# Optimization experiments

Hardware: AMD Instinct MI355X
Metric: run time of the kernel (lower is better)

## Reference

```python
import jax, jax.numpy as jnp
import numpy as np

N, E, G = 100000, 600000, 64  # nodes, edges, graphs
F_IN, W, EPS = 32, 128, 1e-5


def setup_inputs() -> dict:
    key = jax.random.key(0)
    ks = jax.random.split(key, 16)
    p = lambda k, shape: jax.random.normal(k, shape, dtype=jnp.float32) * 0.1
    z = lambda n: jnp.zeros((n,), jnp.float32)
    o = lambda n: jnp.ones((n,), jnp.float32)
    return {
        "x": jax.random.normal(ks[0], (N, F_IN), dtype=jnp.float32),
        "edge_index": jax.random.randint(ks[1], (2, E), 0, N, dtype=jnp.int32),
        "batch": jnp.sort(jax.random.randint(ks[2], (N,), 0, G, dtype=jnp.int32)),
        # GCNConv layers
        "W1": p(ks[3], (F_IN, W)), "b1": z(W),
        "W2": p(ks[4], (W, W)), "b2": z(W),
        # mlp_first: Linear -> BN -> ReLU -> Linear
        "W3": p(ks[5], (W, W)), "b3": z(W), "g1": o(W), "be1": z(W),
        "W4": p(ks[6], (W, W)), "b4": z(W),
        # mlp: Linear -> BN -> ReLU -> Linear
        "W5": p(ks[7], (W, W // 2)), "b5": z(W // 2), "g2": o(W // 2), "be2": z(W // 2),
        "W6": p(ks[8], (W // 2, 1)), "b6": z(1),
    }


def gcn_conv(x, src, dst, Wt, b):
    # PyG GCNConv with add_self_loops=True: D^-1/2 (A+I) D^-1/2 (x W) + b
    h = x @ Wt  # [N, width]
    deg = jax.ops.segment_sum(jnp.ones(src.shape[0], x.dtype), dst, num_segments=N) + 1.0
    dinv = jax.lax.rsqrt(deg)
    norm = dinv[src] * dinv[dst]  # per-edge normalization
    agg = jax.ops.segment_sum(h[src] * norm[:, None], dst, num_segments=N)
    # self-loop term: norm for (i,i) is 1/deg[i]
    return agg + h * (dinv * dinv)[:, None] + b


def batch_norm(x, g, b):
    # training-mode BatchNorm1d (batch stats, biased var)
    mu = x.mean(axis=0)
    var = jnp.mean((x - mu) ** 2, axis=0)
    return (x - mu) * jax.lax.rsqrt(var + EPS) * g + b


def reference(x, edge_index, batch, W1, b1, W2, b2, W3, b3, g1, be1, W4, b4, W5, b5, g2, be2, W6, b6):
    src, dst = edge_index[0], edge_index[1]
    x = jax.nn.relu(gcn_conv(x, src, dst, W1, b1))
    x = jax.nn.relu(gcn_conv(x, src, dst, W2, b2))
    # mlp_first + ReLU
    x = jax.nn.relu(batch_norm(x @ W3 + b3, g1, be1)) @ W4 + b4
    x = jax.nn.relu(x)
    # global max pool over nodes per graph
    x = jax.ops.segment_max(x, batch, num_segments=G)  # [G, width]
    # final mlp
    x = jax.nn.relu(batch_norm(x @ W5 + b5, g2, be2)) @ W6 + b6
    return x[:, 0]
```

## Files before the change

### kernel.cpp

```cpp
#include <hip/hip_runtime.h>

#define N_NODES 100000
#define N_EDGES 600000
#define N_GRAPHS 64
#define EPS 1e-5f
#define SCAN_BLOCKS 391

typedef unsigned short u16;
typedef unsigned int u32;
typedef __attribute__((ext_vector_type(8))) short bf16x8;
typedef __attribute__((ext_vector_type(4))) float f32x4;

__device__ __forceinline__ float bf2f(u16 u) { return __uint_as_float(((u32)u) << 16); }
__device__ __forceinline__ u16 f2bf(float f) {
    u32 u = __float_as_uint(f);
    u += 0x7FFFu + ((u >> 16) & 1u);
    return (u16)(u >> 16);
}
__device__ __forceinline__ float2 bfx2(u32 v) {
    float2 r;
    r.x = __uint_as_float(v << 16);
    r.y = __uint_as_float(v & 0xFFFF0000u);
    return r;
}

#define WS_COUNTS   ((size_t)0)
#define WS_CURSOR   ((size_t)400384)
#define WS_POOLED   ((size_t)800768)
#define WS_BNSUM    ((size_t)833536)
#define WS_BNSUMSQ  ((size_t)834048)
#define WS_FLAG     ((size_t)834560)
#define ZERO_BYTES  ((size_t)835072)
#define WS_OFFSETS  ((size_t)835072)
#define WS_DINV     ((size_t)1235456)
#define WS_DINV2    ((size_t)1635840)
#define WS_SRCS     ((size_t)2036224)
#define WS_ZF       ((size_t)4436736)
#define WS_CANONW   ((size_t)4453120)
#define WS_BUFA     ((size_t)4578560)
#define WS_BUFB     ((size_t)30178560)

#define CW_W1 0
#define CW_B1 4096
#define CW_W2 4224
#define CW_B2 20608
#define CW_W3 20736
#define CW_B3 37120
#define CW_G1 37248
#define CW_BE1 37376
#define CW_W4 37504
#define CW_B4 53888
#define CW_W5 54016
#define CW_B5 62208
#define CW_G2 62272
#define CW_BE2 62336
#define CW_W6 62400
#define CW_B6 62464

__global__ void detect_kernel(const u32* __restrict__ xraw, int* __restrict__ flag) {
    __shared__ int cnt;
    if (threadIdx.x == 0) cnt = 0;
    __syncthreads();
    int c = 0;
    for (int i = threadIdx.x; i < 2048; i += 256) {
        u32 w = xraw[i];
        float a = fabsf(__uint_as_float((w & 0xFFFFu) << 16));
        if (a == 0.f || (a > 1e-8f && a < 1e4f)) c++;
    }
    atomicAdd(&cnt, c);
    __syncthreads();
    if (threadIdx.x == 0) *flag = (cnt > 1024) ? 1 : 0;
}

__global__ void convx_kernel(const void* __restrict__ xsrc, u16* __restrict__ dst,
                             const int* __restrict__ flag) {
    int i = blockIdx.x * 256 + threadIdx.x;
    if (i < N_NODES * 32)
        dst[i] = (*flag) ? ((const u16*)xsrc)[i] : f2bf(((const float*)xsrc)[i]);
}

struct SmallArgs {
    const void* src[16];
    int n[16];
    int off[16];
    int cols[16];
};
__global__ void convs_kernel(SmallArgs a, u16* __restrict__ dst, const int* __restrict__ flag) {
    int i = blockIdx.x * 256 + threadIdx.x;
    int isbf = *flag;
#pragma unroll
    for (int j = 0; j < 16; j++)
        if (i < a.n[j]) {
            u16 v = isbf ? ((const u16*)a.src[j])[i] : f2bf(((const float*)a.src[j])[i]);
            if (a.cols[j] > 0) {
                int k = i / a.cols[j];
                int n = i - k * a.cols[j];
                int Kd = a.n[j] / a.cols[j];
                dst[a.off[j] + n * Kd + k] = v;
            } else {
                dst[a.off[j] + i] = v;
            }
        }
}

__global__ void deg_kernel(const int* __restrict__ dst, int* __restrict__ counts) {
    int e = blockIdx.x * 256 + threadIdx.x;
    if (e < N_EDGES) atomicAdd(&counts[dst[e]], 1);
}

__global__ __launch_bounds__(256) void reduce_kernel(const int* __restrict__ counts,
                                                     int* __restrict__ partials) {
    int i = blockIdx.x * 256 + threadIdx.x;
    int v = (i < N_NODES) ? counts[i] : 0;
    for (int off = 32; off > 0; off >>= 1) v += __shfl_down(v, off, 64);
    __shared__ int wsum[4];
    if ((threadIdx.x & 63) == 0) wsum[threadIdx.x >> 6] = v;
    __syncthreads();
    if (threadIdx.x == 0) partials[blockIdx.x] = wsum[0] + wsum[1] + wsum[2] + wsum[3];
}

__global__ __launch_bounds__(512) void scanpart_kernel(int* __restrict__ partials) {
    __shared__ int sc[512];
    int t = threadIdx.x;
    int v = (t < SCAN_BLOCKS) ? partials[t] : 0;
    sc[t] = v;
    __syncthreads();
    for (int off = 1; off < 512; off <<= 1) {
        int u = (t >= off) ? sc[t - off] : 0;
        __syncthreads();
        sc[t] += u;
        __syncthreads();
    }
    if (t < SCAN_BLOCKS) partials[t] = sc[t] - v;
}

__global__ __launch_bounds__(256) void offsets_kernel(const int* __restrict__ counts,
                                                      const int* __restrict__ partials,
                                                      int* __restrict__ offs,
                                                      float* __restrict__ dinv) {
    int i = blockIdx.x * 256 + threadIdx.x;
    int lane = threadIdx.x & 63, wv = threadIdx.x >> 6;
    int v = (i < N_NODES) ? counts[i] : 0;
    int sv = v;
    for (int off = 1; off < 64; off <<= 1) {
        int u = __shfl_up(sv, off, 64);
        if (lane >= off) sv += u;
    }
    __shared__ int wsum[4];
    if (lane == 63) wsum[wv] = sv;
    __syncthreads();
    int wpre = 0;
    for (int w = 0; w < wv; w++) wpre += wsum[w];
    int excl = sv - v + wpre + partials[blockIdx.x];
    if (i < N_NODES) {
        offs[i] = excl;
        dinv[i] = rsqrtf((float)(v + 1));
    }
    if (i == N_NODES - 1) offs[N_NODES] = excl + v;
}

__global__ void scatter_kernel(const int* __restrict__ src, const int* __restrict__ dst,
                               const int* __restrict__ offs, int* __restrict__ cursor,
                               int* __restrict__ srcs) {
    int e = blockIdx.x * 256 + threadIdx.x;
    if (e < N_EDGES) {
        int d = dst[e];
        int p = offs[d] + atomicAdd(&cursor[d], 1);
        srcs[p] = src[e];
    }
}

template <int K, int IN_MODE, int OUT_MODE>
__global__ __launch_bounds__(256, 3) void mgemm_kernel(
    const u16* __restrict__ A, const u16* __restrict__ Wt, const u16* __restrict__ bias,
    u16* __restrict__ C, const float* __restrict__ scl, const float* __restrict__ shf,
    const float* __restrict__ dscale, float* __restrict__ bn_sum,
    float* __restrict__ bn_sumsq, const int* __restrict__ batch, u32* __restrict__ pooled,
    const int* __restrict__ goffs, const int* __restrict__ gsrcs,
    const float* __restrict__ gdinv, const u16* __restrict__ gbias, int M) {
    constexpr int KP = K + 8;
    constexpr int NKT = K / 32;
    __shared__ __align__(16) u16 Wl[128 * KP];
    __shared__ float csum[128], csumsq[128];

    const int tid = threadIdx.x;
    const int wave = tid >> 6;
    const int lane = tid & 63;
    const int l15 = lane & 15;
    const int quad = lane >> 4;
    const int row0 = blockIdx.x * 128 + wave * 32;

    {
        const u32* g = (const u32*)Wt;
        u32* l = (u32*)Wl;
        for (int i = tid; i < 128 * (K / 2); i += 256) {
            int n = i / (K / 2), j = i - n * (K / 2);
            l[n * (KP / 2) + j] = g[i];
        }
    }
    if (OUT_MODE == 1 && tid < 128) { csum[tid] = 0.f; csumsq[tid] = 0.f; }

    uint4 gr[2][NKT];
    if (IN_MODE == 2) {
#pragma unroll
        for (int rt = 0; rt < 2; rt++) {
            int r = min(row0 + rt * 16 + l15, M - 1);
            int e0 = goffs[r], e1 = goffs[r + 1];
            float ga[NKT][8];
#pragma unroll
            for (int kt = 0; kt < NKT; kt++)
#pragma unroll
                for (int j = 0; j < 8; j++) ga[kt][j] = 0.f;
            for (int e = e0; e < e1; e++) {
                int s = gsrcs[e];
                const u16* hp = A + (size_t)s * K + quad * 8;
#pragma unroll
                for (int kt = 0; kt < NKT; kt++) {
                    uint4 raw = *(const uint4*)(hp + kt * 32);
                    u32 w4[4] = {raw.x, raw.y, raw.z, raw.w};
#pragma unroll
                    for (int t = 0; t < 4; t++) {
                        float2 f = bfx2(w4[t]);
                        ga[kt][2 * t] += f.x;
                        ga[kt][2 * t + 1] += f.y;
                    }
                }
            }
            float di = gdinv[r];
            const u16* op = A + (size_t)r * K + quad * 8;
#pragma unroll
            for (int kt = 0; kt < NKT; kt++) {
                uint4 own = *(const uint4*)(op + kt * 32);
                uint4 bb = *(const uint4*)(gbias + kt * 32 + quad * 8);
                u32 ow[4] = {own.x, own.y, own.z, own.w};
                u32 bw[4] = {bb.x, bb.y, bb.z, bb.w};
                u32 pk[4];
#pragma unroll
                for (int t = 0; t < 4; t++) {
                    float2 fo = bfx2(ow[t]);
                    float2 fb = bfx2(bw[t]);
                    float vx = fmaxf(fmaf(ga[kt][2 * t] + fo.x, di, fb.x), 0.f);
                    float vy = fmaxf(fmaf(ga[kt][2 * t + 1] + fo.y, di, fb.y), 0.f);
                    pk[t] = (u32)f2bf(vx) | ((u32)f2bf(vy) << 16);
                }
                gr[rt][kt] = {pk[0], pk[1], pk[2], pk[3]};
            }
        }
    }
    __syncthreads();

    f32x4 acc[2][8];
#pragma unroll
    for (int rt = 0; rt < 2; rt++)
#pragma unroll
        for (int nt = 0; nt < 8; nt++) acc[rt][nt] = {0.f, 0.f, 0.f, 0.f};

#pragma unroll
    for (int k0 = 0; k0 < K; k0 += 32) {
        bf16x8 af[2];
        if (IN_MODE == 2) {
#pragma unroll
            for (int rt = 0; rt < 2; rt++) af[rt] = __builtin_bit_cast(bf16x8, gr[rt][k0 / 32]);
        } else if (IN_MODE == 0) {
#pragma unroll
            for (int rt = 0; rt < 2; rt++) {
                int r = min(row0 + rt * 16 + l15, M - 1);
                af[rt] = *(const bf16x8*)(A + (size_t)r * K + k0 + quad * 8);
            }
        } else {
            float s8[8], h8[8];
#pragma unroll
            for (int t = 0; t < 8; t++) {
                s8[t] = scl[k0 + quad * 8 + t];
                h8[t] = shf[k0 + quad * 8 + t];
            }
#pragma unroll
            for (int rt = 0; rt < 2; rt++) {
                int r = min(row0 + rt * 16 + l15, M - 1);
                uint4 raw = *(const uint4*)(A + (size_t)r * K + k0 + quad * 8);
                u32 w4[4] = {raw.x, raw.y, raw.z, raw.w};
                bf16x8 tmp;
#pragma unroll
                for (int t = 0; t < 4; t++) {
                    float2 f = bfx2(w4[t]);
                    f.x = fmaxf(fmaf(f.x, s8[2 * t], h8[2 * t]), 0.f);
                    f.y = fmaxf(fmaf(f.y, s8[2 * t + 1], h8[2 * t + 1]), 0.f);
                    tmp[2 * t] = (short)f2bf(f.x);
                    tmp[2 * t + 1] = (short)f2bf(f.y);
                }
                af[rt] = tmp;
            }
        }
#pragma unroll
        for (int nt = 0; nt < 8; nt++) {
            bf16x8 bf = *(const bf16x8*)&Wl[(nt * 16 + l15) * KP + k0 + quad * 8];
            acc[0][nt] = __builtin_amdgcn_mfma_f32_16x16x32_bf16(af[0], bf, acc[0][nt], 0, 0, 0);
            acc[1][nt] = __builtin_amdgcn_mfma_f32_16x16x32_bf16(af[1], bf, acc[1][nt], 0, 0, 0);
        }
    }

    if (OUT_MODE == 0) {
#pragma unroll
        for (int rt = 0; rt < 2; rt++)
#pragma unroll
            for (int i = 0; i < 4; i++) {
                int r = row0 + rt * 16 + quad * 4 + i;
                if (r < M) {
                    float ds = dscale[r];
                    u16* cp = C + (size_t)r * 128 + l15;
#pragma unroll
                    for (int nt = 0; nt < 8; nt++) cp[nt * 16] = f2bf(acc[rt][nt][i] * ds);
                }
            }
    } else if (OUT_MODE == 1) {
        float b[8], s[8], sq[8];
#pragma unroll
        for (int nt = 0; nt < 8; nt++) {
            b[nt] = bf2f(bias[nt * 16 + l15]);
            s[nt] = 0.f;
            sq[nt] = 0.f;
        }
#pragma unroll
        for (int rt = 0; rt < 2; rt++)
#pragma unroll
            for (int i = 0; i < 4; i++) {
                int r = row0 + rt * 16 + quad * 4 + i;
                if (r < M) {
                    u16* cp = C + (size_t)r * 128 + l15;
#pragma unroll
                    for (int nt = 0; nt < 8; nt++) {
                        float v = acc[rt][nt][i] + b[nt];
                        s[nt] += v;
                        sq[nt] += v * v;
                        cp[nt * 16] = f2bf(v);
                    }
                }
            }
#pragma unroll
        for (int nt = 0; nt < 8; nt++) {
            atomicAdd(&csum[nt * 16 + l15], s[nt]);
            atomicAdd(&csumsq[nt * 16 + l15], sq[nt]);
        }
        __syncthreads();
        if (tid < 128) {
            atomicAdd(&bn_sum[tid], csum[tid]);
            atomicAdd(&bn_sumsq[tid], csumsq[tid]);
        }
    } else {
        float b[8];
#pragma unroll
        for (int nt = 0; nt < 8; nt++) b[nt] = bf2f(bias[nt * 16 + l15]);
        float cur[8];
#pragma unroll
        for (int nt = 0; nt < 8; nt++) cur[nt] = 0.f;
        int curg = -1;
#pragma unroll
        for (int rt = 0; rt < 2; rt++)
#pragma unroll
            for (int i = 0; i < 4; i++) {
                int r = row0 + rt * 16 + quad * 4 + i;
                if (r < M) {
                    int g = batch[r];
                    if (g != curg) {
                        if (curg >= 0) {
                            u32* bp = pooled + curg * 128 + l15;
#pragma unroll
                            for (int nt = 0; nt < 8; nt++)
                                if (cur[nt] > 0.f)
                                    atomicMax(&bp[nt * 16], __float_as_uint(cur[nt]));
                        }
                        curg = g;
#pragma unroll
                        for (int nt = 0; nt < 8; nt++) cur[nt] = 0.f;
                    }
#pragma unroll
                    for (int nt = 0; nt < 8; nt++)
                        cur[nt] = fmaxf(cur[nt], fmaxf(acc[rt][nt][i] + b[nt], 0.f));
                }
            }
        if (curg >= 0) {
            u32* bp = pooled + curg * 128 + l15;
#pragma unroll
            for (int nt = 0; nt < 8; nt++)
                if (cur[nt] > 0.f) atomicMax(&bp[nt * 16], __float_as_uint(cur[nt]));
        }
    }
}

__global__ void bnstats_kernel(float* __restrict__ bn_sum, float* __restrict__ bn_sumsq,
                               const u16* __restrict__ g1, const u16* __restrict__ be1) {
    int c = threadIdx.x;
    if (c < 128) {
        float mu = bn_sum[c] / (float)N_NODES;
        float var = bn_sumsq[c] / (float)N_NODES - mu * mu;
        float rstd = rsqrtf(var + EPS);
        float sc = rstd * bf2f(g1[c]);
        bn_sum[c] = sc;
        bn_sumsq[c] = bf2f(be1[c]) - mu * sc;
    }
}

__global__ __launch_bounds__(256) void head1_kernel(const u32* __restrict__ pooled,
                                                    const u16* __restrict__ W5,
                                                    const u16* __restrict__ b5,
                                                    float* __restrict__ zf) {
    __shared__ float red[4][64];
    int g = blockIdx.x;
    int c = threadIdx.x & 63;
    int kq = threadIdx.x >> 6;
    const u32* prow = pooled + g * 128;
    float p = 0.f;
    for (int k = kq * 32; k < kq * 32 + 32; k++)
        p = fmaf(__uint_as_float(prow[k]), bf2f(W5[k * 64 + c]), p);
    red[kq][c] = p;
    __syncthreads();
    if (kq == 0) zf[g * 64 + c] = red[0][c] + red[1][c] + red[2][c] + red[3][c] + bf2f(b5[c]);
}

__global__ __launch_bounds__(64) void head2_kernel(const float* __restrict__ zf,
                                                   const u16* __restrict__ g2,
                                                   const u16* __restrict__ be2,
                                                   const u16* __restrict__ W6,
                                                   const u16* __restrict__ b6,
                                                   void* __restrict__ outv,
                                                   const int* __restrict__ flag) {
    __shared__ float Z[64][65];
    __shared__ float sc[64], sh[64], w6[64];
    int t = threadIdx.x;
    for (int idx = t; idx < 4096; idx += 64) Z[idx >> 6][idx & 63] = zf[idx];
    w6[t] = bf2f(W6[t]);
    __syncthreads();
    {
        float s = 0.f, sq = 0.f;
        for (int g = 0; g < 64; g++) {
            float v = Z[g][t];
            s += v;
            sq += v * v;
        }
        float mu = s * (1.f / 64.f);
        float var = sq * (1.f / 64.f) - mu * mu;
        float rstd = rsqrtf(var + EPS);
        float scale = rstd * bf2f(g2[t]);
        sc[t] = scale;
        sh[t] = bf2f(be2[t]) - mu * scale;
    }
    __syncthreads();
    float o = 0.f;
    for (int c = 0; c < 64; c++)
        o = fmaf(fmaxf(fmaf(Z[t][c], sc[c], sh[c]), 0.f), w6[c], o);
    float res = o + bf2f(b6[0]);
    if (*flag)
        ((u16*)outv)[t] = f2bf(res);
    else
        ((float*)outv)[t] = res;
}

extern "C" void kernel_launch(void* const* d_in, const int* in_sizes, int n_in, void* d_out,
                              int out_size, void* d_ws, size_t ws_size, hipStream_t stream) {
    const void* x = d_in[0];
    const int* ei = (const int*)d_in[1];
    const int* bat = (const int*)d_in[2];

    char* ws = (char*)d_ws;
    int* counts = (int*)(ws + WS_COUNTS);
    int* cursor = (int*)(ws + WS_CURSOR);
    u32* pooled = (u32*)(ws + WS_POOLED);
    float* bnsum = (float*)(ws + WS_BNSUM);
    float* bnssq = (float*)(ws + WS_BNSUMSQ);
    int* flag = (int*)(ws + WS_FLAG);
    int* offs = (int*)(ws + WS_OFFSETS);
    float* dinv = (float*)(ws + WS_DINV);
    int* partials = (int*)(ws + WS_DINV2);
    int* srcs = (int*)(ws + WS_SRCS);
    float* zf = (float*)(ws + WS_ZF);
    u16* cw = (u16*)(ws + WS_CANONW);
    u16* bufA = (u16*)(ws + WS_BUFA);
    u16* bufB = (u16*)(ws + WS_BUFB);
    u16* canonx = bufB;

    const int* esrc = ei;
    const int* edst = ei + N_EDGES;

    hipMemsetAsync(ws, 0, ZERO_BYTES, stream);
    detect_kernel<<<1, 256, 0, stream>>>((const u32*)x, flag);

    convx_kernel<<<(N_NODES * 32 + 255) / 256, 256, 0, stream>>>(x, canonx, flag);
    SmallArgs sa;
    const int cw_off[16] = {CW_W1, CW_B1, CW_W2, CW_B2, CW_W3, CW_B3, CW_G1, CW_BE1,
                            CW_W4, CW_B4, CW_W5, CW_B5, CW_G2, CW_BE2, CW_W6, CW_B6};
    const int cw_n[16] = {4096, 128, 16384, 128, 16384, 128, 128, 128,
                          16384, 128, 8192, 64, 64, 64, 64, 1};
    const int cw_c[16] = {128, 0, 128, 0, 128, 0, 0, 0, 128, 0, 0, 0, 0, 0, 0, 0};
    for (int j = 0; j < 16; j++) {
        sa.src[j] = d_in[3 + j];
        sa.n[j] = cw_n[j];
        sa.off[j] = cw_off[j];
        sa.cols[j] = cw_c[j];
    }
    convs_kernel<<<64, 256, 0, stream>>>(sa, cw, flag);

    deg_kernel<<<(N_EDGES + 255) / 256, 256, 0, stream>>>(edst, counts);
    reduce_kernel<<<SCAN_BLOCKS, 256, 0, stream>>>(counts, partials);
    scanpart_kernel<<<1, 512, 0, stream>>>(partials);
    offsets_kernel<<<SCAN_BLOCKS, 256, 0, stream>>>(counts, partials, offs, dinv);
    scatter_kernel<<<(N_EDGES + 255) / 256, 256, 0, stream>>>(esrc, edst, offs, cursor, srcs);

    const int gb = (N_NODES + 127) / 128;
    mgemm_kernel<32, 0, 0><<<gb, 256, 0, stream>>>(canonx, cw + CW_W1, nullptr, bufA, nullptr,
                                                   nullptr, dinv, nullptr, nullptr, nullptr,
                                                   nullptr, nullptr, nullptr, nullptr, nullptr,
                                                   N_NODES);
    mgemm_kernel<128, 2, 0><<<gb, 256, 0, stream>>>(bufA, cw + CW_W2, nullptr, bufB, nullptr,
                                                    nullptr, dinv, nullptr, nullptr, nullptr,
                                                    nullptr, offs, srcs, dinv, cw + CW_B1,
                                                    N_NODES);
    mgemm_kernel<128, 2, 1><<<gb, 256, 0, stream>>>(bufB, cw + CW_W3, cw + CW_B3, bufA, nullptr,
                                                    nullptr, nullptr, bnsum, bnssq, nullptr,
                                                    nullptr, offs, srcs, dinv, cw + CW_B2,
                                                    N_NODES);
    bnstats_kernel<<<1, 128, 0, stream>>>(bnsum, bnssq, cw + CW_G1, cw + CW_BE1);
    mgemm_kernel<128, 1, 2><<<gb, 256, 0, stream>>>(bufA, cw + CW_W4, cw + CW_B4, nullptr, bnsum,
                                                    bnssq, nullptr, nullptr, nullptr, bat,
                                                    pooled, nullptr, nullptr, nullptr, nullptr,
                                                    N_NODES);
    head1_kernel<<<N_GRAPHS, 256, 0, stream>>>(pooled, cw + CW_W5, cw + CW_B5, zf);
    head2_kernel<<<1, 64, 0, stream>>>(zf, cw + CW_G2, cw + CW_BE2, cw + CW_W6, cw + CW_B6,
                                       d_out, flag);
}
```

Before: 366.1 us.

## Fuse input conversion into first GEMM, unroll gather, merge head kernels

Removes the separate x-conversion kernel, so the first GEMM reads raw x directly and converts fp32 to bf16 on load according to the dtype flag. Unrolls the neighbor-gather loop by two so each lane has more independent loads in flight. Merges the two head kernels into a single 1024-thread block, which drops a launch and the global round trip through zf but leaves only one block doing the W5 matmul serially. The goals are fewer kernel launches and one less full pass over x, at the cost of extra registers in the gather loop.

```diff
diff --git a/kernel.cpp b/kernel.cpp
--- a/kernel.cpp
+++ b/kernel.cpp
@@ -72,13 +72,6 @@
     if (threadIdx.x == 0) *flag = (cnt > 1024) ? 1 : 0;
 }
 
-__global__ void convx_kernel(const void* __restrict__ xsrc, u16* __restrict__ dst,
-                             const int* __restrict__ flag) {
-    int i = blockIdx.x * 256 + threadIdx.x;
-    if (i < N_NODES * 32)
-        dst[i] = (*flag) ? ((const u16*)xsrc)[i] : f2bf(((const float*)xsrc)[i]);
-}
-
 struct SmallArgs {
     const void* src[16];
     int n[16];
@@ -177,7 +170,8 @@
     const float* __restrict__ dscale, float* __restrict__ bn_sum,
     float* __restrict__ bn_sumsq, const int* __restrict__ batch, u32* __restrict__ pooled,
     const int* __restrict__ goffs, const int* __restrict__ gsrcs,
-    const float* __restrict__ gdinv, const u16* __restrict__ gbias, int M) {
+    const float* __restrict__ gdinv, const u16* __restrict__ gbias,
+    const int* __restrict__ gflag, int M) {
     constexpr int KP = K + 8;
     constexpr int NKT = K / 32;
     __shared__ __align__(16) u16 Wl[128 * KP];
@@ -211,7 +205,32 @@
             for (int kt = 0; kt < NKT; kt++)
 #pragma unroll
                 for (int j = 0; j < 8; j++) ga[kt][j] = 0.f;
-            for (int e = e0; e < e1; e++) {
+            int e = e0;
+            for (; e + 1 < e1; e += 2) {
+                int sa = gsrcs[e];
+                int sb = gsrcs[e + 1];
+                const u16* hpa = A + (size_t)sa * K + quad * 8;
+                const u16* hpb = A + (size_t)sb * K + quad * 8;
+                uint4 ra[NKT], rb[NKT];
+#pragma unroll
+                for (int kt = 0; kt < NKT; kt++) {
+                    ra[kt] = *(const uint4*)(hpa + kt * 32);
+                    rb[kt] = *(const uint4*)(hpb + kt * 32);
+                }
+#pragma unroll
+                for (int kt = 0; kt < NKT; kt++) {
+                    u32 wa[4] = {ra[kt].x, ra[kt].y, ra[kt].z, ra[kt].w};
+                    u32 wb[4] = {rb[kt].x, rb[kt].y, rb[kt].z, rb[kt].w};
+#pragma unroll
+                    for (int t = 0; t < 4; t++) {
+                        float2 fa = bfx2(wa[t]);
+                        float2 fb = bfx2(wb[t]);
+                        ga[kt][2 * t] += fa.x + fb.x;
+                        ga[kt][2 * t + 1] += fa.y + fb.y;
+                    }
+                }
+            }
+            if (e < e1) {
                 int s = gsrcs[e];
                 const u16* hp = A + (size_t)s * K + quad * 8;
 #pragma unroll
@@ -255,6 +274,8 @@
 #pragma unroll
         for (int nt = 0; nt < 8; nt++) acc[rt][nt] = {0.f, 0.f, 0.f, 0.f};
 
+    const bool xisbf = (IN_MODE == 3) ? (*gflag != 0) : true;
+
 #pragma unroll
     for (int k0 = 0; k0 < K; k0 += 32) {
         bf16x8 af[2];
@@ -266,6 +287,24 @@
             for (int rt = 0; rt < 2; rt++) {
                 int r = min(row0 + rt * 16 + l15, M - 1);
                 af[rt] = *(const bf16x8*)(A + (size_t)r * K + k0 + quad * 8);
+            }
+        } else if (IN_MODE == 3) {
+#pragma unroll
+            for (int rt = 0; rt < 2; rt++) {
+                int r = min(row0 + rt * 16 + l15, M - 1);
+                if (xisbf) {
+                    af[rt] = *(const bf16x8*)(A + (size_t)r * K + k0 + quad * 8);
+                } else {
+                    const float* xf = (const float*)A;
+                    float4 f0 = *(const float4*)(xf + (size_t)r * K + k0 + quad * 8);
+                    float4 f1 = *(const float4*)(xf + (size_t)r * K + k0 + quad * 8 + 4);
+                    bf16x8 tmp;
+                    tmp[0] = (short)f2bf(f0.x); tmp[1] = (short)f2bf(f0.y);
+                    tmp[2] = (short)f2bf(f0.z); tmp[3] = (short)f2bf(f0.w);
+                    tmp[4] = (short)f2bf(f1.x); tmp[5] = (short)f2bf(f1.y);
+                    tmp[6] = (short)f2bf(f1.z); tmp[7] = (short)f2bf(f1.w);
+                    af[rt] = tmp;
+                }
             }
         } else {
             float s8[8], h8[8];
@@ -400,37 +439,28 @@
     }
 }
 
-__global__ __launch_bounds__(256) void head1_kernel(const u32* __restrict__ pooled,
+__global__ __launch_bounds__(1024) void head_kernel(const u32* __restrict__ pooled,
                                                     const u16* __restrict__ W5,
                                                     const u16* __restrict__ b5,
-                                                    float* __restrict__ zf) {
-    __shared__ float red[4][64];
-    int g = blockIdx.x;
-    int c = threadIdx.x & 63;
-    int kq = threadIdx.x >> 6;
-    const u32* prow = pooled + g * 128;
-    float p = 0.f;
-    for (int k = kq * 32; k < kq * 32 + 32; k++)
-        p = fmaf(__uint_as_float(prow[k]), bf2f(W5[k * 64 + c]), p);
-    red[kq][c] = p;
-    __syncthreads();
-    if (kq == 0) zf[g * 64 + c] = red[0][c] + red[1][c] + red[2][c] + red[3][c] + bf2f(b5[c]);
-}
-
-__global__ __launch_bounds__(64) void head2_kernel(const float* __restrict__ zf,
-                                                   const u16* __restrict__ g2,
-                                                   const u16* __restrict__ be2,
-                                                   const u16* __restrict__ W6,
-                                                   const u16* __restrict__ b6,
-                                                   void* __restrict__ outv,
-                                                   const int* __restrict__ flag) {
+                                                    const u16* __restrict__ g2,
+                                                    const u16* __restrict__ be2,
+                                                    const u16* __restrict__ W6,
+                                                    const u16* __restrict__ b6,
+                                                    void* __restrict__ outv,
+                                                    const int* __restrict__ flag) {
     __shared__ float Z[64][65];
-    __shared__ float sc[64], sh[64], w6[64];
+    __shared__ float sc[64], sh[64];
     int t = threadIdx.x;
-    for (int idx = t; idx < 4096; idx += 64) Z[idx >> 6][idx & 63] = zf[idx];
-    w6[t] = bf2f(W6[t]);
-    __syncthreads();
-    {
+    for (int idx = t; idx < 4096; idx += 1024) {
+        int g = idx >> 6, c = idx & 63;
+        const u32* prow = pooled + g * 128;
+        float p = bf2f(b5[c]);
+        for (int k = 0; k < 128; k++)
+            p = fmaf(__uint_as_float(prow[k]), bf2f(W5[k * 64 + c]), p);
+        Z[g][c] = p;
+    }
+    __syncthreads();
+    if (t < 64) {
         float s = 0.f, sq = 0.f;
         for (int g = 0; g < 64; g++) {
             float v = Z[g][t];
@@ -439,20 +469,20 @@
         }
         float mu = s * (1.f / 64.f);
         float var = sq * (1.f / 64.f) - mu * mu;
-        float rstd = rsqrtf(var + EPS);
-        float scale = rstd * bf2f(g2[t]);
+        float scale = rsqrtf(var + EPS) * bf2f(g2[t]);
         sc[t] = scale;
         sh[t] = bf2f(be2[t]) - mu * scale;
     }
     __syncthreads();
-    float o = 0.f;
-    for (int c = 0; c < 64; c++)
-        o = fmaf(fmaxf(fmaf(Z[t][c], sc[c], sh[c]), 0.f), w6[c], o);
-    float res = o + bf2f(b6[0]);
-    if (*flag)
-        ((u16*)outv)[t] = f2bf(res);
-    else
-        ((float*)outv)[t] = res;
+    if (t < 64) {
+        float o = bf2f(b6[0]);
+        for (int c = 0; c < 64; c++)
+            o = fmaf(fmaxf(fmaf(Z[t][c], sc[c], sh[c]), 0.f), bf2f(W6[c]), o);
+        if (*flag)
+            ((u16*)outv)[t] = f2bf(o);
+        else
+            ((float*)outv)[t] = o;
+    }
 }
 
 extern "C" void kernel_launch(void* const* d_in, const int* in_sizes, int n_in, void* d_out,
@@ -472,11 +502,9 @@
     float* dinv = (float*)(ws + WS_DINV);
     int* partials = (int*)(ws + WS_DINV2);
     int* srcs = (int*)(ws + WS_SRCS);
-    float* zf = (float*)(ws + WS_ZF);
     u16* cw = (u16*)(ws + WS_CANONW);
     u16* bufA = (u16*)(ws + WS_BUFA);
     u16* bufB = (u16*)(ws + WS_BUFB);
-    u16* canonx = bufB;
 
     const int* esrc = ei;
     const int* edst = ei + N_EDGES;
@@ -484,7 +512,6 @@
     hipMemsetAsync(ws, 0, ZERO_BYTES, stream);
     detect_kernel<<<1, 256, 0, stream>>>((const u32*)x, flag);
 
-    convx_kernel<<<(N_NODES * 32 + 255) / 256, 256, 0, stream>>>(x, canonx, flag);
     SmallArgs sa;
     const int cw_off[16] = {CW_W1, CW_B1, CW_W2, CW_B2, CW_W3, CW_B3, CW_G1, CW_BE1,
                             CW_W4, CW_B4, CW_W5, CW_B5, CW_G2, CW_BE2, CW_W6, CW_B6};
@@ -506,24 +533,23 @@
     scatter_kernel<<<(N_EDGES + 255) / 256, 256, 0, stream>>>(esrc, edst, offs, cursor, srcs);
 
     const int gb = (N_NODES + 127) / 128;
-    mgemm_kernel<32, 0, 0><<<gb, 256, 0, stream>>>(canonx, cw + CW_W1, nullptr, bufA, nullptr,
-                                                   nullptr, dinv, nullptr, nullptr, nullptr,
+    mgemm_kernel<32, 3, 0><<<gb, 256, 0, stream>>>((const u16*)x, cw + CW_W1, nullptr, bufA,
+                                                   nullptr, nullptr, dinv, nullptr, nullptr,
                                                    nullptr, nullptr, nullptr, nullptr, nullptr,
-                                                   N_NODES);
+                                                   nullptr, flag, N_NODES);
     mgemm_kernel<128, 2, 0><<<gb, 256, 0, stream>>>(bufA, cw + CW_W2, nullptr, bufB, nullptr,
                                                     nullptr, dinv, nullptr, nullptr, nullptr,
                                                     nullptr, offs, srcs, dinv, cw + CW_B1,
-                                                    N_NODES);
+                                                    nullptr, N_NODES);
     mgemm_kernel<128, 2, 1><<<gb, 256, 0, stream>>>(bufB, cw + CW_W3, cw + CW_B3, bufA, nullptr,
                                                     nullptr, nullptr, bnsum, bnssq, nullptr,
                                                     nullptr, offs, srcs, dinv, cw + CW_B2,
-                                                    N_NODES);
+                                                    nullptr, N_NODES);
     bnstats_kernel<<<1, 128, 0, stream>>>(bnsum, bnssq, cw + CW_G1, cw + CW_BE1);
     mgemm_kernel<128, 1, 2><<<gb, 256, 0, stream>>>(bufA, cw + CW_W4, cw + CW_B4, nullptr, bnsum,
                                                     bnssq, nullptr, nullptr, nullptr, bat,
                                                     pooled, nullptr, nullptr, nullptr, nullptr,
-                                                    N_NODES);
-    head1_kernel<<<N_GRAPHS, 256, 0, stream>>>(pooled, cw + CW_W5, cw + CW_B5, zf);
-    head2_kernel<<<1, 64, 0, stream>>>(zf, cw + CW_G2, cw + CW_BE2, cw + CW_W6, cw + CW_B6,
-                                       d_out, flag);
-}
+                                                    nullptr, N_NODES);
+    head_kernel<<<1, 1024, 0, stream>>>(pooled, cw + CW_W5, cw + CW_B5, cw + CW_G2, cw + CW_BE2,
+                                        cw + CW_W6, cw + CW_B6, d_out, flag);
+}
```

Result: slower. 394.2 us (+7.7%).

## Renumber nodes by in-degree bins and fuse x conversion into first GEMM

Applied to the files above, without the earlier changes.

Adds a counting-sort permutation of nodes by in-degree (bins, binscan, perm kernels), builds CSR and all intermediate buffers in the permuted order, and un-permutes only when writing the BN-stage output. The aim is to give rows within a wave similar neighbor counts so the gather-fused GEMMs see less load imbalance and divergence. It also removes the separate x conversion kernel by reading x (fp32 or bf16) directly through the permutation inside the first GEMM. The cost is three extra small kernels, indirect reads through the permutation, and scattered output writes.

```diff
diff --git a/kernel.cpp b/kernel.cpp
--- a/kernel.cpp
+++ b/kernel.cpp
@@ -30,15 +30,17 @@
 #define WS_BNSUM    ((size_t)833536)
 #define WS_BNSUMSQ  ((size_t)834048)
 #define WS_FLAG     ((size_t)834560)
-#define ZERO_BYTES  ((size_t)835072)
-#define WS_OFFSETS  ((size_t)835072)
-#define WS_DINV     ((size_t)1235456)
-#define WS_DINV2    ((size_t)1635840)
-#define WS_SRCS     ((size_t)2036224)
-#define WS_ZF       ((size_t)4436736)
-#define WS_CANONW   ((size_t)4453120)
-#define WS_BUFA     ((size_t)4578560)
-#define WS_BUFB     ((size_t)30178560)
+#define WS_BINOFF   ((size_t)835072)
+#define WS_BINCUR   ((size_t)835584)
+#define WS_PARTIALS ((size_t)836096)
+#define ZERO_BYTES  ((size_t)838144)
+#define WS_OFFSETS  ((size_t)838144)
+#define WS_DINV     ((size_t)1238528)
+#define WS_ORIG     ((size_t)1638912)
+#define WS_SRCS     ((size_t)2039296)
+#define WS_CANONW   ((size_t)4439552)
+#define WS_BUFA     ((size_t)4564992)
+#define WS_BUFB     ((size_t)30164992)
 
 #define CW_W1 0
 #define CW_B1 4096
@@ -72,13 +74,6 @@
     if (threadIdx.x == 0) *flag = (cnt > 1024) ? 1 : 0;
 }
 
-__global__ void convx_kernel(const void* __restrict__ xsrc, u16* __restrict__ dst,
-                             const int* __restrict__ flag) {
-    int i = blockIdx.x * 256 + threadIdx.x;
-    if (i < N_NODES * 32)
-        dst[i] = (*flag) ? ((const u16*)xsrc)[i] : f2bf(((const float*)xsrc)[i]);
-}
-
 struct SmallArgs {
     const void* src[16];
     int n[16];
@@ -108,10 +103,60 @@
     if (e < N_EDGES) atomicAdd(&counts[dst[e]], 1);
 }
 
+__global__ __launch_bounds__(256) void bins_kernel(const int* __restrict__ counts,
+                                                   int* __restrict__ binoff) {
+    __shared__ int lh[64];
+    if (threadIdx.x < 64) lh[threadIdx.x] = 0;
+    __syncthreads();
+    int i = blockIdx.x * 256 + threadIdx.x;
+    if (i < N_NODES) atomicAdd(&lh[min(counts[i], 63)], 1);
+    __syncthreads();
+    if (threadIdx.x < 64 && lh[threadIdx.x]) atomicAdd(&binoff[threadIdx.x], lh[threadIdx.x]);
+}
+
+__global__ __launch_bounds__(64) void binscan_kernel(int* __restrict__ binoff) {
+    int t = threadIdx.x;
+    int v = binoff[t];
+    int sv = v;
+    for (int off = 1; off < 64; off <<= 1) {
+        int u = __shfl_up(sv, off, 64);
+        if (t >= off) sv += u;
+    }
+    binoff[t] = sv - v;
+}
+
+__global__ __launch_bounds__(256) void perm_kernel(const int* __restrict__ counts,
+                                                   const int* __restrict__ binoff,
+                                                   int* __restrict__ bincur,
+                                                   int* __restrict__ pos,
+                                                   int* __restrict__ orig) {
+    __shared__ int lh[64];
+    __shared__ int gbase[64];
+    if (threadIdx.x < 64) lh[threadIdx.x] = 0;
+    __syncthreads();
+    int i = blockIdx.x * 256 + threadIdx.x;
+    int b = 0, rl = 0;
+    bool valid = i < N_NODES;
+    if (valid) {
+        b = min(counts[i], 63);
+        rl = atomicAdd(&lh[b], 1);
+    }
+    __syncthreads();
+    if (threadIdx.x < 64 && lh[threadIdx.x])
+        gbase[threadIdx.x] = atomicAdd(&bincur[threadIdx.x], lh[threadIdx.x]);
+    __syncthreads();
+    if (valid) {
+        int p = binoff[b] + gbase[b] + rl;
+        pos[i] = p;
+        orig[p] = i;
+    }
+}
+
 __global__ __launch_bounds__(256) void reduce_kernel(const int* __restrict__ counts,
+                                                     const int* __restrict__ orig,
                                                      int* __restrict__ partials) {
     int i = blockIdx.x * 256 + threadIdx.x;
-    int v = (i < N_NODES) ? counts[i] : 0;
+    int v = (i < N_NODES) ? counts[orig[i]] : 0;
     for (int off = 32; off > 0; off >>= 1) v += __shfl_down(v, off, 64);
     __shared__ int wsum[4];
     if ((threadIdx.x & 63) == 0) wsum[threadIdx.x >> 6] = v;
@@ -135,12 +180,13 @@
 }
 
 __global__ __launch_bounds__(256) void offsets_kernel(const int* __restrict__ counts,
+                                                      const int* __restrict__ orig,
                                                       const int* __restrict__ partials,
                                                       int* __restrict__ offs,
                                                       float* __restrict__ dinv) {
     int i = blockIdx.x * 256 + threadIdx.x;
     int lane = threadIdx.x & 63, wv = threadIdx.x >> 6;
-    int v = (i < N_NODES) ? counts[i] : 0;
+    int v = (i < N_NODES) ? counts[orig[i]] : 0;
     int sv = v;
     for (int off = 1; off < 64; off <<= 1) {
         int u = __shfl_up(sv, off, 64);
@@ -160,13 +206,13 @@
 }
 
 __global__ void scatter_kernel(const int* __restrict__ src, const int* __restrict__ dst,
-                               const int* __restrict__ offs, int* __restrict__ cursor,
-                               int* __restrict__ srcs) {
+                               const int* __restrict__ pos, const int* __restrict__ offs,
+                               int* __restrict__ cursor, int* __restrict__ srcs) {
     int e = blockIdx.x * 256 + threadIdx.x;
     if (e < N_EDGES) {
-        int d = dst[e];
-        int p = offs[d] + atomicAdd(&cursor[d], 1);
-        srcs[p] = src[e];
+        int pd = pos[dst[e]];
+        int p = offs[pd] + atomicAdd(&cursor[pd], 1);
+        srcs[p] = pos[src[e]];
     }
 }
 
@@ -177,7 +223,8 @@
     const float* __restrict__ dscale, float* __restrict__ bn_sum,
     float* __restrict__ bn_sumsq, const int* __restrict__ batch, u32* __restrict__ pooled,
     const int* __restrict__ goffs, const int* __restrict__ gsrcs,
-    const float* __restrict__ gdinv, const u16* __restrict__ gbias, int M) {
+    const float* __restrict__ gdinv, const u16* __restrict__ gbias,
+    const int* __restrict__ gflag, const int* __restrict__ gorig, int M) {
     constexpr int KP = K + 8;
     constexpr int NKT = K / 32;
     __shared__ __align__(16) u16 Wl[128 * KP];
@@ -255,6 +302,8 @@
 #pragma unroll
         for (int nt = 0; nt < 8; nt++) acc[rt][nt] = {0.f, 0.f, 0.f, 0.f};
 
+    const bool xisbf = (IN_MODE == 3) ? (*gflag != 0) : true;
+
 #pragma unroll
     for (int k0 = 0; k0 < K; k0 += 32) {
         bf16x8 af[2];
@@ -266,6 +315,25 @@
             for (int rt = 0; rt < 2; rt++) {
                 int r = min(row0 + rt * 16 + l15, M - 1);
                 af[rt] = *(const bf16x8*)(A + (size_t)r * K + k0 + quad * 8);
+            }
+        } else if (IN_MODE == 3) {
+#pragma unroll
+            for (int rt = 0; rt < 2; rt++) {
+                int r = min(row0 + rt * 16 + l15, M - 1);
+                int ro = gorig[r];
+                if (xisbf) {
+                    af[rt] = *(const bf16x8*)(A + (size_t)ro * K + k0 + quad * 8);
+                } else {
+                    const float* xf = (const float*)A;
+                    float4 f0 = *(const float4*)(xf + (size_t)ro * K + k0 + quad * 8);
+                    float4 f1 = *(const float4*)(xf + (size_t)ro * K + k0 + quad * 8 + 4);
+                    bf16x8 tmp;
+                    tmp[0] = (short)f2bf(f0.x); tmp[1] = (short)f2bf(f0.y);
+                    tmp[2] = (short)f2bf(f0.z); tmp[3] = (short)f2bf(f0.w);
+                    tmp[4] = (short)f2bf(f1.x); tmp[5] = (short)f2bf(f1.y);
+                    tmp[6] = (short)f2bf(f1.z); tmp[7] = (short)f2bf(f1.w);
+                    af[rt] = tmp;
+                }
             }
         } else {
             float s8[8], h8[8];
@@ -326,7 +394,8 @@
             for (int i = 0; i < 4; i++) {
                 int r = row0 + rt * 16 + quad * 4 + i;
                 if (r < M) {
-                    u16* cp = C + (size_t)r * 128 + l15;
+                    int rs = gorig[r];
+                    u16* cp = C + (size_t)rs * 128 + l15;
 #pragma unroll
                     for (int nt = 0; nt < 8; nt++) {
                         float v = acc[rt][nt][i] + b[nt];
@@ -468,15 +537,18 @@
     float* bnsum = (float*)(ws + WS_BNSUM);
     float* bnssq = (float*)(ws + WS_BNSUMSQ);
     int* flag = (int*)(ws + WS_FLAG);
+    int* binoff = (int*)(ws + WS_BINOFF);
+    int* bincur = (int*)(ws + WS_BINCUR);
+    int* partials = (int*)(ws + WS_PARTIALS);
     int* offs = (int*)(ws + WS_OFFSETS);
     float* dinv = (float*)(ws + WS_DINV);
-    int* partials = (int*)(ws + WS_DINV2);
+    int* orig = (int*)(ws + WS_ORIG);
     int* srcs = (int*)(ws + WS_SRCS);
-    float* zf = (float*)(ws + WS_ZF);
     u16* cw = (u16*)(ws + WS_CANONW);
     u16* bufA = (u16*)(ws + WS_BUFA);
     u16* bufB = (u16*)(ws + WS_BUFB);
-    u16* canonx = bufB;
+    int* pos = (int*)(ws + WS_BUFB);
+    float* zf = (float*)(ws + WS_SRCS);
 
     const int* esrc = ei;
     const int* edst = ei + N_EDGES;
@@ -484,7 +556,6 @@
     hipMemsetAsync(ws, 0, ZERO_BYTES, stream);
     detect_kernel<<<1, 256, 0, stream>>>((const u32*)x, flag);
 
-    convx_kernel<<<(N_NODES * 32 + 255) / 256, 256, 0, stream>>>(x, canonx, flag);
     SmallArgs sa;
     const int cw_off[16] = {CW_W1, CW_B1, CW_W2, CW_B2, CW_W3, CW_B3, CW_G1, CW_BE1,
                             CW_W4, CW_B4, CW_W5, CW_B5, CW_G2, CW_BE2, CW_W6, CW_B6};
@@ -500,29 +571,33 @@
     convs_kernel<<<64, 256, 0, stream>>>(sa, cw, flag);
 
     deg_kernel<<<(N_EDGES + 255) / 256, 256, 0, stream>>>(edst, counts);
-    reduce_kernel<<<SCAN_BLOCKS, 256, 0, stream>>>(counts, partials);
+    bins_kernel<<<SCAN_BLOCKS, 256, 0, stream>>>(counts, binoff);
+    binscan_kernel<<<1, 64, 0, stream>>>(binoff);
+    perm_kernel<<<SCAN_BLOCKS, 256, 0, stream>>>(counts, binoff, bincur, pos, orig);
+    reduce_kernel<<<SCAN_BLOCKS, 256, 0, stream>>>(counts, orig, partials);
     scanpart_kernel<<<1, 512, 0, stream>>>(partials);
-    offsets_kernel<<<SCAN_BLOCKS, 256, 0, stream>>>(counts, partials, offs, dinv);
-    scatter_kernel<<<(N_EDGES + 255) / 256, 256, 0, stream>>>(esrc, edst, offs, cursor, srcs);
+    offsets_kernel<<<SCAN_BLOCKS, 256, 0, stream>>>(counts, orig, partials, offs, dinv);
+    scatter_kernel<<<(N_EDGES + 255) / 256, 256, 0, stream>>>(esrc, edst, pos, offs, cursor,
+                                                              srcs);
 
     const int gb = (N_NODES + 127) / 128;
-    mgemm_kernel<32, 0, 0><<<gb, 256, 0, stream>>>(canonx, cw + CW_W1, nullptr, bufA, nullptr,
-                                                   nullptr, dinv, nullptr, nullptr, nullptr,
+    mgemm_kernel<32, 3, 0><<<gb, 256, 0, stream>>>((const u16*)x, cw + CW_W1, nullptr, bufA,
+                                                   nullptr, nullptr, dinv, nullptr, nullptr,
                                                    nullptr, nullptr, nullptr, nullptr, nullptr,
-                                                   N_NODES);
+                                                   nullptr, flag, orig, N_NODES);
     mgemm_kernel<128, 2, 0><<<gb, 256, 0, stream>>>(bufA, cw + CW_W2, nullptr, bufB, nullptr,
                                                     nullptr, dinv, nullptr, nullptr, nullptr,
                                                     nullptr, offs, srcs, dinv, cw + CW_B1,
-                                                    N_NODES);
+                                                    nullptr, nullptr, N_NODES);
     mgemm_kernel<128, 2, 1><<<gb, 256, 0, stream>>>(bufB, cw + CW_W3, cw + CW_B3, bufA, nullptr,
                                                     nullptr, nullptr, bnsum, bnssq, nullptr,
                                                     nullptr, offs, srcs, dinv, cw + CW_B2,
-                                                    N_NODES);
+                                                    nullptr, orig, N_NODES);
     bnstats_kernel<<<1, 128, 0, stream>>>(bnsum, bnssq, cw + CW_G1, cw + CW_BE1);
     mgemm_kernel<128, 1, 2><<<gb, 256, 0, stream>>>(bufA, cw + CW_W4, cw + CW_B4, nullptr, bnsum,
                                                     bnssq, nullptr, nullptr, nullptr, bat,
                                                     pooled, nullptr, nullptr, nullptr, nullptr,
-                                                    N_NODES);
+                                                    nullptr, nullptr, N_NODES);
     head1_kernel<<<N_GRAPHS, 256, 0, stream>>>(pooled, cw + CW_W5, cw + CW_B5, zf);
     head2_kernel<<<1, 64, 0, stream>>>(zf, cw + CW_G2, cw + CW_BE2, cw + CW_W6, cw + CW_B6,
                                        d_out, flag);
```

Result: slower. 375.2 us (+2.5%).
